# Performance work log

Measured on AMD Instinct MI355X. Metric: run time of the kernel, lower is better.

Reference implementation:

```python
import jax, jax.numpy as jnp
import numpy as np

B = 64
L_IN = 4001
L_CONV = 998  # (4001-10)//4 + 1
D = 1000
EPS = 1e-5


def _convlin(x, cw, cb, lw, lb):
    # x: (B,1,4001), cw: (1,1,10), lw: (1000,998)
    y = jax.lax.conv_general_dilated(
        x, cw, window_strides=(4,), padding='VALID',
        dimension_numbers=('NCH', 'OIH', 'NCH')) + cb[None, :, None]  # (B,1,998)
    y = y @ lw.T + lb  # (B,1,1000)
    return jax.nn.relu(y)


def setup_inputs() -> dict:
    key = jax.random.key(0)
    ks = jax.random.split(key, 24)
    f32 = jnp.float32
    inp = {
        'x': jax.random.normal(ks[0], (B, 1, L_IN), dtype=f32),
        'bn_gamma': jnp.ones((L_IN,), f32),
        'bn_beta': jnp.zeros((L_IN,), f32),
        'bn_mean': jax.random.normal(ks[1], (L_IN,), f32) * 0.1,
        'bn_var': jax.random.uniform(ks[2], (L_IN,), f32, 0.5, 1.5),
        'conv_w_q': jax.random.normal(ks[3], (1, 1, 10), f32) * 0.3,
        'conv_b_q': jax.random.normal(ks[4], (1,), f32) * 0.1,
        'lin_w_q': jax.random.normal(ks[5], (D, L_CONV), f32) * (1.0 / np.sqrt(L_CONV)),
        'lin_b_q': jax.random.normal(ks[6], (D,), f32) * 0.02,
        'conv_w_k': jax.random.normal(ks[7], (1, 1, 10), f32) * 0.3,
        'conv_b_k': jax.random.normal(ks[8], (1,), f32) * 0.1,
        'lin_w_k': jax.random.normal(ks[9], (D, L_CONV), f32) * (1.0 / np.sqrt(L_CONV)),
        'lin_b_k': jax.random.normal(ks[10], (D,), f32) * 0.02,
        'conv_w_v': jax.random.normal(ks[11], (1, 1, 10), f32) * 0.3,
        'conv_b_v': jax.random.normal(ks[12], (1,), f32) * 0.1,
        'lin_w_v': jax.random.normal(ks[13], (D, L_CONV), f32) * (1.0 / np.sqrt(L_CONV)),
        'lin_b_v': jax.random.normal(ks[14], (D,), f32) * 0.02,
        'in_proj_w': jax.random.normal(ks[15], (3, 1), f32),
        'in_proj_b': jax.random.normal(ks[16], (3,), f32) * 0.02,
        'out_proj_w': jax.random.normal(ks[17], (1, 1), f32),
        'out_proj_b': jax.random.normal(ks[18], (1,), f32) * 0.02,
        'out_w': jax.random.normal(ks[19], (D, D), f32) * (1.0 / np.sqrt(D)),
        'out_b': jax.random.normal(ks[20], (D,), f32) * 0.02,
    }
    return inp


def reference(x, bn_gamma, bn_beta, bn_mean, bn_var,
              conv_w_q, conv_b_q, lin_w_q, lin_b_q,
              conv_w_k, conv_b_k, lin_w_k, lin_b_k,
              conv_w_v, conv_b_v, lin_w_v, lin_b_v,
              in_proj_w, in_proj_b, out_proj_w, out_proj_b,
              out_w, out_b):
    # BatchNorm1d over last dim (eval mode, running stats); x: (B,1,4001)
    xn = (x - bn_mean[None, None, :]) * jax.lax.rsqrt(bn_var[None, None, :] + EPS)
    xn = xn * bn_gamma[None, None, :] + bn_beta[None, None, :]

    Q = _convlin(xn, conv_w_q, conv_b_q, lin_w_q, lin_b_q)[:, 0, :]  # (B,1000)
    K = _convlin(xn, conv_w_k, conv_b_k, lin_w_k, lin_b_k)[:, 0, :]
    V = _convlin(xn, conv_w_v, conv_b_v, lin_w_v, lin_b_v)[:, 0, :]

    # MHA with embed_dim=1, num_heads=1 -> scalar in-projections, scale = 1
    q = Q * in_proj_w[0, 0] + in_proj_b[0]  # (B,1000)
    k = K * in_proj_w[1, 0] + in_proj_b[1]
    v = V * in_proj_w[2, 0] + in_proj_b[2]

    scores = q[:, :, None] * k[:, None, :]  # (B,1000,1000)
    attn = jax.nn.softmax(scores, axis=-1)
    ctx = jnp.einsum('bqk,bk->bq', attn, v)  # (B,1000)
    ctx = ctx * out_proj_w[0, 0] + out_proj_b[0]

    out = ctx[:, None, :] @ out_w.T + out_b  # (B,1,1000)
    return out
```

## Files before the change

kernel.cpp:

```cpp
#include <hip/hip_runtime.h>
#include <math.h>

#define NB 64
#define LIN 4001
#define LC 998
#define ND 1000
#define EPSBN 1e-5f

#define CK 96
#define NCH_LIN 11
#define NCH_OUT 11

#define OFF_CONVT 0u
#define OFF_PP    191616u
#define OFF_CF    2354304u
#define OFF_OP    2418304u

__global__ __launch_bounds__(256) void k_bnconv(
    const float* __restrict__ x,
    const float* __restrict__ g, const float* __restrict__ be,
    const float* __restrict__ mu, const float* __restrict__ va,
    const float* __restrict__ cwq, const float* __restrict__ cbq,
    const float* __restrict__ cwk, const float* __restrict__ cbk,
    const float* __restrict__ cwv, const float* __restrict__ cbv,
    float* __restrict__ convT)
{
    int j = blockIdx.x * 256 + threadIdx.x;
    int b = blockIdx.y;
    if (j >= LC) return;
    const float* xb = x + (size_t)b * LIN + 4 * j;
    float aq = 0.f, ak = 0.f, av = 0.f;
#pragma unroll
    for (int t = 0; t < 10; ++t) {
        int i = 4 * j + t;
        float s  = g[i] * rsqrtf(va[i] + EPSBN);
        float xn = (xb[t] - mu[i]) * s + be[i];
        aq = fmaf(xn, cwq[t], aq);
        ak = fmaf(xn, cwk[t], ak);
        av = fmaf(xn, cwv[t], av);
    }
    convT[((size_t)0 * LC + j) * 64 + b] = aq + cbq[0];
    convT[((size_t)1 * LC + j) * 64 + b] = ak + cbk[0];
    convT[((size_t)2 * LC + j) * 64 + b] = av + cbv[0];
}

__device__ __forceinline__ void gemm_tile(
    const float* __restrict__ Asrc,
    const float* __restrict__ Brow,
    int ldB, int dgb, int j0, int jc,
    float* __restrict__ Pt,
    float* lds)
{
    float* ldsC = lds;
    float* ldsW = lds + 6144;
    int tid  = threadIdx.x;
    int lane = tid & 63;
    int w    = tid >> 6;
    int b0   = (lane & 7) << 3;
    int d0   = (lane >> 3) << 3;

    {
        const float4* src = (const float4*)Asrc;
        float4* dst = (float4*)ldsC;
        for (int t = tid; t < jc * 16; t += 256) dst[t] = src[t];
    }
    for (int idx = tid; idx < 3072; idx += 256) {
        int dd = idx / 48, j2 = idx % 48;
        int dg = dgb + dd;
        float2 v = make_float2(0.f, 0.f);
        if (dg < ND && 2 * j2 < jc)
            v = *(const float2*)(Brow + (size_t)dg * ldB + j0 + 2 * j2);
        ldsW[dd * 97 + 2 * j2]     = v.x;
        ldsW[dd * 97 + 2 * j2 + 1] = v.y;
    }
    __syncthreads();

    float acc[8][8];
#pragma unroll
    for (int i = 0; i < 8; ++i)
#pragma unroll
        for (int jx = 0; jx < 8; ++jx) acc[i][jx] = 0.f;

    int js = (jc * w) >> 2;
    int je = (jc * (w + 1)) >> 2;
    for (int jj = js; jj < je; ++jj) {
        float4 c0 = *(const float4*)(ldsC + jj * 64 + b0);
        float4 c1 = *(const float4*)(ldsC + jj * 64 + b0 + 4);
        float cv[8] = {c0.x, c0.y, c0.z, c0.w, c1.x, c1.y, c1.z, c1.w};
        float wv[8];
#pragma unroll
        for (int r = 0; r < 8; ++r) wv[r] = ldsW[(d0 + r) * 97 + jj];
#pragma unroll
        for (int i = 0; i < 8; ++i)
#pragma unroll
            for (int jx = 0; jx < 8; ++jx)
                acc[i][jx] = fmaf(cv[i], wv[jx], acc[i][jx]);
    }
    __syncthreads();

    for (int p = 0; p < 2; ++p) {
        float* red = lds + w * 2304;
#pragma unroll
        for (int i = 0; i < 8; ++i)
            *(float4*)(red + (b0 + i) * 36 + (d0 >> 1)) =
                make_float4(acc[i][4*p], acc[i][4*p+1], acc[i][4*p+2], acc[i][4*p+3]);
        __syncthreads();
        for (int t = tid; t < 512; t += 256) {
            int bb = t >> 3, gg = t & 7;
            int o = bb * 36 + 4 * gg;
            float4 a0 = *(const float4*)(lds + o);
            float4 a1 = *(const float4*)(lds + 2304 + o);
            float4 a2 = *(const float4*)(lds + 4608 + o);
            float4 a3 = *(const float4*)(lds + 6912 + o);
            float4 s;
            s.x = a0.x + a1.x + a2.x + a3.x;
            s.y = a0.y + a1.y + a2.y + a3.y;
            s.z = a0.z + a1.z + a2.z + a3.z;
            s.w = a0.w + a1.w + a2.w + a3.w;
            *(float4*)(Pt + bb * 64 + 8 * gg + 4 * p) = s;
        }
        __syncthreads();
    }
}

__global__ __launch_bounds__(256) void k_lin(
    const float* __restrict__ convT,
    const float* __restrict__ lwq, const float* __restrict__ lwk,
    const float* __restrict__ lwv,
    float* __restrict__ Pp)
{
    __shared__ float lds[12352];
    int dgb   = blockIdx.x * 64;
    int which = blockIdx.y;
    int chunk = blockIdx.z;
    int j0 = chunk * CK;
    int jc = (LC - j0 < CK) ? (LC - j0) : CK;
    const float* lw = (which == 0) ? lwq : ((which == 1) ? lwk : lwv);
    const float* Asrc = convT + ((size_t)which * LC + j0) * 64;
    float* Pt = Pp + (((size_t)chunk * 3 + which) * 16 + blockIdx.x) * 4096;
    gemm_tile(Asrc, lw, LC, dgb, j0, jc, Pt, lds);
}

__global__ __launch_bounds__(256) void k_attn(
    const float* __restrict__ Pp,
    const float* __restrict__ lbq, const float* __restrict__ lbk,
    const float* __restrict__ lbv,
    const float* __restrict__ ipw, const float* __restrict__ ipb,
    const float* __restrict__ opw, const float* __restrict__ opb,
    float* __restrict__ cfT)
{
    __shared__ float skv[2000];
    __shared__ float sql[128];
    __shared__ float sd[512];
    __shared__ float sn[512];
    __shared__ float rmax[4];
    __shared__ float rmin[4];
    const float LOG2E = 1.4426950408889634f;
    int tid  = threadIdx.x;
    int b    = blockIdx.y;
    int i0   = blockIdx.x * 128;
    int w    = tid >> 6;
    int lane = tid & 63;

    float ipw1 = ipw[1], ipb1 = ipb[1];
    float ipw2 = ipw[2], ipb2 = ipb[2];

    for (int j = tid; j < ND; j += 256) {
        int it = j >> 6, il = j & 63;
        size_t base = ((size_t)it) * 4096 + (b << 6) + il;
        float sk = 0.f, sv = 0.f;
        for (int c = 0; c < NCH_LIN; ++c) {
            sk += Pp[((size_t)(c * 3 + 1) * 16) * 4096 + base];
            sv += Pp[((size_t)(c * 3 + 2) * 16) * 4096 + base];
        }
        float yk = fmaxf(sk + lbk[j], 0.f) * ipw1 + ipb1;
        float yv = fmaxf(sv + lbv[j], 0.f) * ipw2 + ipb2;
        skv[2 * j]     = yk * LOG2E;
        skv[2 * j + 1] = yv;
    }
    if (tid < 128) {
        int i = i0 + tid;
        float sq = 0.f;
        if (i < ND) {
            int it = i >> 6, il = i & 63;
            size_t base = ((size_t)it) * 4096 + (b << 6) + il;
            for (int c = 0; c < NCH_LIN; ++c)
                sq += Pp[((size_t)(c * 3 + 0) * 16) * 4096 + base];
            sq = fmaxf(sq + lbq[i], 0.f) * ipw[0] + ipb[0];
        }
        sql[tid] = sq;
    }
    __syncthreads();

    float km = -INFINITY, kn = INFINITY;
    for (int j = tid; j < ND; j += 256) {
        float f = skv[2 * j];
        km = fmaxf(km, f);
        kn = fminf(kn, f);
    }
#pragma unroll
    for (int off = 1; off < 64; off <<= 1) {
        km = fmaxf(km, __shfl_xor(km, off));
        kn = fminf(kn, __shfl_xor(kn, off));
    }
    if (lane == 0) { rmax[w] = km; rmin[w] = kn; }
    __syncthreads();
    km = fmaxf(fmaxf(rmax[0], rmax[1]), fmaxf(rmax[2], rmax[3]));
    kn = fminf(fminf(rmin[0], rmin[1]), fminf(rmin[2], rmin[3]));

    float q0 = sql[lane];
    float q1 = sql[64 + lane];
    float m0 = (q0 >= 0.f) ? q0 * km : q0 * kn;
    float m1 = (q1 >= 0.f) ? q1 * km : q1 * kn;
    const float2* kv2 = (const float2*)skv;
    int jb = w * 250;
    float d0a = 0.f, n0a = 0.f, d1a = 0.f, n1a = 0.f;
#pragma unroll 2
    for (int jl = 0; jl < 250; ++jl) {
        float2 f = kv2[jb + jl];
        float e0 = exp2f(fmaf(q0, f.x, -m0));
        float e1 = exp2f(fmaf(q1, f.x, -m1));
        d0a += e0; n0a = fmaf(e0, f.y, n0a);
        d1a += e1; n1a = fmaf(e1, f.y, n1a);
    }
    sd[w * 128 + lane]      = d0a;
    sd[w * 128 + 64 + lane] = d1a;
    sn[w * 128 + lane]      = n0a;
    sn[w * 128 + 64 + lane] = n1a;
    __syncthreads();

    if (tid < 128) {
        int i = i0 + tid;
        if (i < ND) {
            float dt = sd[tid] + sd[128 + tid] + sd[256 + tid] + sd[384 + tid];
            float nt = sn[tid] + sn[128 + tid] + sn[256 + tid] + sn[384 + tid];
            cfT[(size_t)i * 64 + b] = (nt / dt) * opw[0] + opb[0];
        }
    }
}

__global__ __launch_bounds__(256) void k_out(
    const float* __restrict__ cfT, const float* __restrict__ W,
    float* __restrict__ Op)
{
    __shared__ float lds[12352];
    int egb   = blockIdx.x * 64;
    int chunk = blockIdx.y;
    int j0 = chunk * CK;
    int jc = (ND - j0 < CK) ? (ND - j0) : CK;
    const float* Asrc = cfT + (size_t)j0 * 64;
    float* Pt = Op + ((size_t)chunk * 16 + blockIdx.x) * 4096;
    gemm_tile(Asrc, W, ND, egb, j0, jc, Pt, lds);
}

__global__ __launch_bounds__(256) void k_fin(
    const float* __restrict__ Op, const float* __restrict__ outb,
    float* __restrict__ out)
{
    int e = blockIdx.x * 256 + threadIdx.x;
    int b = blockIdx.y;
    if (e >= ND) return;
    float s = outb[e];
    size_t cell = ((size_t)(e >> 6)) * 4096 + (b << 6) + (e & 63);
    for (int c = 0; c < NCH_OUT; ++c)
        s += Op[(size_t)c * 16 * 4096 + cell];
    out[(size_t)b * ND + e] = s;
}

extern "C" void kernel_launch(void* const* d_in, const int* in_sizes, int n_in,
                              void* d_out, int out_size, void* d_ws, size_t ws_size,
                              hipStream_t stream)
{
    const float* x    = (const float*)d_in[0];
    const float* g    = (const float*)d_in[1];
    const float* be   = (const float*)d_in[2];
    const float* mu   = (const float*)d_in[3];
    const float* va   = (const float*)d_in[4];
    const float* cwq  = (const float*)d_in[5];
    const float* cbq  = (const float*)d_in[6];
    const float* lwq  = (const float*)d_in[7];
    const float* lbq  = (const float*)d_in[8];
    const float* cwk  = (const float*)d_in[9];
    const float* cbk  = (const float*)d_in[10];
    const float* lwk  = (const float*)d_in[11];
    const float* lbk  = (const float*)d_in[12];
    const float* cwv  = (const float*)d_in[13];
    const float* cbv  = (const float*)d_in[14];
    const float* lwv  = (const float*)d_in[15];
    const float* lbv  = (const float*)d_in[16];
    const float* ipw  = (const float*)d_in[17];
    const float* ipb  = (const float*)d_in[18];
    const float* opw  = (const float*)d_in[19];
    const float* opb  = (const float*)d_in[20];
    const float* W    = (const float*)d_in[21];
    const float* outb = (const float*)d_in[22];

    float* ws    = (float*)d_ws;
    float* convT = ws + OFF_CONVT;
    float* Pp    = ws + OFF_PP;
    float* cfT   = ws + OFF_CF;
    float* Op    = ws + OFF_OP;
    float* out   = (float*)d_out;

    k_bnconv<<<dim3(4, 64), 256, 0, stream>>>(x, g, be, mu, va,
                                              cwq, cbq, cwk, cbk, cwv, cbv, convT);
    k_lin  <<<dim3(16, 3, NCH_LIN), 256, 0, stream>>>(convT, lwq, lwk, lwv, Pp);
    k_attn <<<dim3(8, 64), 256, 0, stream>>>(Pp, lbq, lbk, lbv, ipw, ipb,
                                             opw, opb, cfT);
    k_out  <<<dim3(16, NCH_OUT), 256, 0, stream>>>(cfT, W, Op);
    k_fin  <<<dim3(4, 64), 256, 0, stream>>>(Op, outb, out);
}
```

Measured before the change: 174.5 us.

## Fuse all five stages into one cooperative persistent kernel with grid syncs

Replaces the five separate kernel launches with a single cooperative kernel of 512 blocks that runs each stage and separates them with grid.sync(). The K-chunk size grows from 96 to 104, so there are 10 partial chunks instead of 11. The attention-input reduction now runs as its own grid-wide stage that writes q and the interleaved k/v into global scratch, so attention blocks no longer each redo the partial-sum reduction. The aim is to remove launch gaps and redundant reductions, at the cost of grid-barrier overhead and fewer active blocks in the GEMM stages.

```diff
diff --git a/kernel.cpp b/kernel.cpp
--- a/kernel.cpp
+++ b/kernel.cpp
@@ -1,5 +1,8 @@
 #include <hip/hip_runtime.h>
+#include <hip/hip_cooperative_groups.h>
 #include <math.h>
+
+namespace cg = cooperative_groups;
 
 #define NB 64
 #define LIN 4001
@@ -7,42 +10,28 @@
 #define ND 1000
 #define EPSBN 1e-5f
 
-#define CK 96
-#define NCH_LIN 11
-#define NCH_OUT 11
+#define CK 104
+#define NCH_LIN 10
+#define NCH_OUT 10
+#define T_LIN 480
+#define T_OUT 160
+#define GRID 512
 
 #define OFF_CONVT 0u
 #define OFF_PP    191616u
-#define OFF_CF    2354304u
-#define OFF_OP    2418304u
-
-__global__ __launch_bounds__(256) void k_bnconv(
-    const float* __restrict__ x,
-    const float* __restrict__ g, const float* __restrict__ be,
-    const float* __restrict__ mu, const float* __restrict__ va,
-    const float* __restrict__ cwq, const float* __restrict__ cbq,
-    const float* __restrict__ cwk, const float* __restrict__ cbk,
-    const float* __restrict__ cwv, const float* __restrict__ cbv,
-    float* __restrict__ convT)
-{
-    int j = blockIdx.x * 256 + threadIdx.x;
-    int b = blockIdx.y;
-    if (j >= LC) return;
-    const float* xb = x + (size_t)b * LIN + 4 * j;
-    float aq = 0.f, ak = 0.f, av = 0.f;
-#pragma unroll
-    for (int t = 0; t < 10; ++t) {
-        int i = 4 * j + t;
-        float s  = g[i] * rsqrtf(va[i] + EPSBN);
-        float xn = (xb[t] - mu[i]) * s + be[i];
-        aq = fmaf(xn, cwq[t], aq);
-        ak = fmaf(xn, cwk[t], ak);
-        av = fmaf(xn, cwv[t], av);
-    }
-    convT[((size_t)0 * LC + j) * 64 + b] = aq + cbq[0];
-    convT[((size_t)1 * LC + j) * 64 + b] = ak + cbk[0];
-    convT[((size_t)2 * LC + j) * 64 + b] = av + cbv[0];
-}
+#define OFF_Q     2157696u
+#define OFF_KV    2221696u
+#define OFF_CF    2352768u
+#define OFF_OP    2416768u
+
+struct Params {
+    const float *x, *g, *be, *mu, *va;
+    const float *cwq, *cbq, *lwq, *lbq;
+    const float *cwk, *cbk, *lwk, *lbk;
+    const float *cwv, *cbv, *lwv, *lbv;
+    const float *ipw, *ipb, *opw, *opb, *W, *outb;
+    float *convT, *Pp, *qg, *kvg, *cfT, *Op, *out;
+};
 
 __device__ __forceinline__ void gemm_tile(
     const float* __restrict__ Asrc,
@@ -52,7 +41,7 @@
     float* lds)
 {
     float* ldsC = lds;
-    float* ldsW = lds + 6144;
+    float* ldsW = lds + 6656;
     int tid  = threadIdx.x;
     int lane = tid & 63;
     int w    = tid >> 6;
@@ -64,14 +53,14 @@
         float4* dst = (float4*)ldsC;
         for (int t = tid; t < jc * 16; t += 256) dst[t] = src[t];
     }
-    for (int idx = tid; idx < 3072; idx += 256) {
-        int dd = idx / 48, j2 = idx % 48;
+    for (int idx = tid; idx < 3328; idx += 256) {
+        int dd = idx / 52, j2 = idx % 52;
         int dg = dgb + dd;
         float2 v = make_float2(0.f, 0.f);
         if (dg < ND && 2 * j2 < jc)
             v = *(const float2*)(Brow + (size_t)dg * ldB + j0 + 2 * j2);
-        ldsW[dd * 97 + 2 * j2]     = v.x;
-        ldsW[dd * 97 + 2 * j2 + 1] = v.y;
+        ldsW[dd * 105 + 2 * j2]     = v.x;
+        ldsW[dd * 105 + 2 * j2 + 1] = v.y;
     }
     __syncthreads();
 
@@ -89,7 +78,7 @@
         float cv[8] = {c0.x, c0.y, c0.z, c0.w, c1.x, c1.y, c1.z, c1.w};
         float wv[8];
 #pragma unroll
-        for (int r = 0; r < 8; ++r) wv[r] = ldsW[(d0 + r) * 97 + jj];
+        for (int r = 0; r < 8; ++r) wv[r] = ldsW[(d0 + r) * 105 + jj];
 #pragma unroll
         for (int i = 0; i < 8; ++i)
 #pragma unroll
@@ -123,190 +112,211 @@
     }
 }
 
-__global__ __launch_bounds__(256) void k_lin(
-    const float* __restrict__ convT,
-    const float* __restrict__ lwq, const float* __restrict__ lwk,
-    const float* __restrict__ lwv,
-    float* __restrict__ Pp)
+__global__ __launch_bounds__(256, 2) void k_all(Params p)
 {
-    __shared__ float lds[12352];
-    int dgb   = blockIdx.x * 64;
-    int which = blockIdx.y;
-    int chunk = blockIdx.z;
-    int j0 = chunk * CK;
-    int jc = (LC - j0 < CK) ? (LC - j0) : CK;
-    const float* lw = (which == 0) ? lwq : ((which == 1) ? lwk : lwv);
-    const float* Asrc = convT + ((size_t)which * LC + j0) * 64;
-    float* Pt = Pp + (((size_t)chunk * 3 + which) * 16 + blockIdx.x) * 4096;
-    gemm_tile(Asrc, lw, LC, dgb, j0, jc, Pt, lds);
-}
-
-__global__ __launch_bounds__(256) void k_attn(
-    const float* __restrict__ Pp,
-    const float* __restrict__ lbq, const float* __restrict__ lbk,
-    const float* __restrict__ lbv,
-    const float* __restrict__ ipw, const float* __restrict__ ipb,
-    const float* __restrict__ opw, const float* __restrict__ opb,
-    float* __restrict__ cfT)
-{
-    __shared__ float skv[2000];
-    __shared__ float sql[128];
-    __shared__ float sd[512];
-    __shared__ float sn[512];
-    __shared__ float rmax[4];
-    __shared__ float rmin[4];
-    const float LOG2E = 1.4426950408889634f;
-    int tid  = threadIdx.x;
-    int b    = blockIdx.y;
-    int i0   = blockIdx.x * 128;
-    int w    = tid >> 6;
-    int lane = tid & 63;
-
-    float ipw1 = ipw[1], ipb1 = ipb[1];
-    float ipw2 = ipw[2], ipb2 = ipb[2];
-
-    for (int j = tid; j < ND; j += 256) {
-        int it = j >> 6, il = j & 63;
-        size_t base = ((size_t)it) * 4096 + (b << 6) + il;
-        float sk = 0.f, sv = 0.f;
-        for (int c = 0; c < NCH_LIN; ++c) {
-            sk += Pp[((size_t)(c * 3 + 1) * 16) * 4096 + base];
-            sv += Pp[((size_t)(c * 3 + 2) * 16) * 4096 + base];
-        }
-        float yk = fmaxf(sk + lbk[j], 0.f) * ipw1 + ipb1;
-        float yv = fmaxf(sv + lbv[j], 0.f) * ipw2 + ipb2;
-        skv[2 * j]     = yk * LOG2E;
-        skv[2 * j + 1] = yv;
-    }
-    if (tid < 128) {
-        int i = i0 + tid;
-        float sq = 0.f;
-        if (i < ND) {
+    __shared__ float lds[13376];
+    cg::grid_group grid = cg::this_grid();
+    const int tid = threadIdx.x;
+    const int bid = blockIdx.x;
+    const int gsz = GRID * 256;
+    const int gtid = bid * 256 + tid;
+
+    {
+        int idx = gtid;
+        if (idx < LC * NB) {
+            int j = idx % LC, b = idx / LC;
+            const float* xb = p.x + (size_t)b * LIN + 4 * j;
+            float aq = 0.f, ak = 0.f, av = 0.f;
+#pragma unroll
+            for (int t = 0; t < 10; ++t) {
+                int i = 4 * j + t;
+                float s  = p.g[i] * rsqrtf(p.va[i] + EPSBN);
+                float xn = (xb[t] - p.mu[i]) * s + p.be[i];
+                aq = fmaf(xn, p.cwq[t], aq);
+                ak = fmaf(xn, p.cwk[t], ak);
+                av = fmaf(xn, p.cwv[t], av);
+            }
+            p.convT[((size_t)0 * LC + j) * 64 + b] = aq + p.cbq[0];
+            p.convT[((size_t)1 * LC + j) * 64 + b] = ak + p.cbk[0];
+            p.convT[((size_t)2 * LC + j) * 64 + b] = av + p.cbv[0];
+        }
+    }
+    grid.sync();
+
+    if (bid < T_LIN) {
+        int t = bid;
+        int dx = t & 15;
+        int which = (t >> 4) % 3;
+        int chunk = t / 48;
+        int j0 = chunk * CK;
+        int jc = (LC - j0 < CK) ? (LC - j0) : CK;
+        const float* lw = (which == 0) ? p.lwq : ((which == 1) ? p.lwk : p.lwv);
+        const float* Asrc = p.convT + ((size_t)which * LC + j0) * 64;
+        float* Pt = p.Pp + (((size_t)chunk * 3 + which) * 16 + dx) * 4096;
+        gemm_tile(Asrc, lw, LC, dx * 64, j0, jc, Pt, lds);
+    }
+    grid.sync();
+
+    {
+        int idx = gtid;
+        if (idx < NB * ND) {
+            int i = idx % ND, b = idx / ND;
             int it = i >> 6, il = i & 63;
             size_t base = ((size_t)it) * 4096 + (b << 6) + il;
-            for (int c = 0; c < NCH_LIN; ++c)
-                sq += Pp[((size_t)(c * 3 + 0) * 16) * 4096 + base];
-            sq = fmaxf(sq + lbq[i], 0.f) * ipw[0] + ipb[0];
-        }
-        sql[tid] = sq;
-    }
-    __syncthreads();
-
-    float km = -INFINITY, kn = INFINITY;
-    for (int j = tid; j < ND; j += 256) {
-        float f = skv[2 * j];
-        km = fmaxf(km, f);
-        kn = fminf(kn, f);
-    }
-#pragma unroll
-    for (int off = 1; off < 64; off <<= 1) {
-        km = fmaxf(km, __shfl_xor(km, off));
-        kn = fminf(kn, __shfl_xor(kn, off));
-    }
-    if (lane == 0) { rmax[w] = km; rmin[w] = kn; }
-    __syncthreads();
-    km = fmaxf(fmaxf(rmax[0], rmax[1]), fmaxf(rmax[2], rmax[3]));
-    kn = fminf(fminf(rmin[0], rmin[1]), fminf(rmin[2], rmin[3]));
-
-    float q0 = sql[lane];
-    float q1 = sql[64 + lane];
-    float m0 = (q0 >= 0.f) ? q0 * km : q0 * kn;
-    float m1 = (q1 >= 0.f) ? q1 * km : q1 * kn;
-    const float2* kv2 = (const float2*)skv;
-    int jb = w * 250;
-    float d0a = 0.f, n0a = 0.f, d1a = 0.f, n1a = 0.f;
+            float s0 = 0.f, s1 = 0.f, s2 = 0.f;
+            for (int c = 0; c < NCH_LIN; ++c) {
+                size_t o = ((size_t)c * 3 * 16) * 4096 + base;
+                s0 += p.Pp[o];
+                s1 += p.Pp[o + 16 * 4096];
+                s2 += p.Pp[o + 32 * 4096];
+            }
+            const float LOG2E = 1.4426950408889634f;
+            float yq = fmaxf(s0 + p.lbq[i], 0.f) * p.ipw[0] + p.ipb[0];
+            float yk = fmaxf(s1 + p.lbk[i], 0.f) * p.ipw[1] + p.ipb[1];
+            float yv = fmaxf(s2 + p.lbv[i], 0.f) * p.ipw[2] + p.ipb[2];
+            p.qg[(size_t)b * ND + i] = yq;
+            p.kvg[(size_t)b * 2048 + 2 * i]     = yk * LOG2E;
+            p.kvg[(size_t)b * 2048 + 2 * i + 1] = yv;
+        }
+    }
+    grid.sync();
+
+    {
+        float* skv  = lds;
+        float* sql  = lds + 2000;
+        float* sd   = lds + 2128;
+        float* sn   = lds + 2640;
+        float* rmax = lds + 3152;
+        float* rmin = lds + 3156;
+        int t  = bid;
+        int i0 = (t & 7) * 128;
+        int b  = t >> 3;
+        int w    = tid >> 6;
+        int lane = tid & 63;
+
+        {
+            const float4* src = (const float4*)(p.kvg + (size_t)b * 2048);
+            float4* dst = (float4*)skv;
+            for (int tt = tid; tt < 500; tt += 256) dst[tt] = src[tt];
+        }
+        if (tid < 128) {
+            int i = i0 + tid;
+            sql[tid] = (i < ND) ? p.qg[(size_t)b * ND + i] : 0.f;
+        }
+        __syncthreads();
+
+        float km = -INFINITY, kn = INFINITY;
+        for (int j = tid; j < ND; j += 256) {
+            float f = skv[2 * j];
+            km = fmaxf(km, f);
+            kn = fminf(kn, f);
+        }
+#pragma unroll
+        for (int off = 1; off < 64; off <<= 1) {
+            km = fmaxf(km, __shfl_xor(km, off));
+            kn = fminf(kn, __shfl_xor(kn, off));
+        }
+        if (lane == 0) { rmax[w] = km; rmin[w] = kn; }
+        __syncthreads();
+        km = fmaxf(fmaxf(rmax[0], rmax[1]), fmaxf(rmax[2], rmax[3]));
+        kn = fminf(fminf(rmin[0], rmin[1]), fminf(rmin[2], rmin[3]));
+
+        float q0 = sql[lane];
+        float q1 = sql[64 + lane];
+        float m0 = (q0 >= 0.f) ? q0 * km : q0 * kn;
+        float m1 = (q1 >= 0.f) ? q1 * km : q1 * kn;
+        const float2* kv2 = (const float2*)skv;
+        int jb = w * 250;
+        float d0a = 0.f, n0a = 0.f, d1a = 0.f, n1a = 0.f;
 #pragma unroll 2
-    for (int jl = 0; jl < 250; ++jl) {
-        float2 f = kv2[jb + jl];
-        float e0 = exp2f(fmaf(q0, f.x, -m0));
-        float e1 = exp2f(fmaf(q1, f.x, -m1));
-        d0a += e0; n0a = fmaf(e0, f.y, n0a);
-        d1a += e1; n1a = fmaf(e1, f.y, n1a);
-    }
-    sd[w * 128 + lane]      = d0a;
-    sd[w * 128 + 64 + lane] = d1a;
-    sn[w * 128 + lane]      = n0a;
-    sn[w * 128 + 64 + lane] = n1a;
-    __syncthreads();
-
-    if (tid < 128) {
-        int i = i0 + tid;
-        if (i < ND) {
-            float dt = sd[tid] + sd[128 + tid] + sd[256 + tid] + sd[384 + tid];
-            float nt = sn[tid] + sn[128 + tid] + sn[256 + tid] + sn[384 + tid];
-            cfT[(size_t)i * 64 + b] = (nt / dt) * opw[0] + opb[0];
-        }
-    }
-}
-
-__global__ __launch_bounds__(256) void k_out(
-    const float* __restrict__ cfT, const float* __restrict__ W,
-    float* __restrict__ Op)
-{
-    __shared__ float lds[12352];
-    int egb   = blockIdx.x * 64;
-    int chunk = blockIdx.y;
-    int j0 = chunk * CK;
-    int jc = (ND - j0 < CK) ? (ND - j0) : CK;
-    const float* Asrc = cfT + (size_t)j0 * 64;
-    float* Pt = Op + ((size_t)chunk * 16 + blockIdx.x) * 4096;
-    gemm_tile(Asrc, W, ND, egb, j0, jc, Pt, lds);
-}
-
-__global__ __launch_bounds__(256) void k_fin(
-    const float* __restrict__ Op, const float* __restrict__ outb,
-    float* __restrict__ out)
-{
-    int e = blockIdx.x * 256 + threadIdx.x;
-    int b = blockIdx.y;
-    if (e >= ND) return;
-    float s = outb[e];
-    size_t cell = ((size_t)(e >> 6)) * 4096 + (b << 6) + (e & 63);
-    for (int c = 0; c < NCH_OUT; ++c)
-        s += Op[(size_t)c * 16 * 4096 + cell];
-    out[(size_t)b * ND + e] = s;
+        for (int jl = 0; jl < 250; ++jl) {
+            float2 f = kv2[jb + jl];
+            float e0 = exp2f(fmaf(q0, f.x, -m0));
+            float e1 = exp2f(fmaf(q1, f.x, -m1));
+            d0a += e0; n0a = fmaf(e0, f.y, n0a);
+            d1a += e1; n1a = fmaf(e1, f.y, n1a);
+        }
+        sd[w * 128 + lane]      = d0a;
+        sd[w * 128 + 64 + lane] = d1a;
+        sn[w * 128 + lane]      = n0a;
+        sn[w * 128 + 64 + lane] = n1a;
+        __syncthreads();
+
+        if (tid < 128) {
+            int i = i0 + tid;
+            if (i < ND) {
+                float dt = sd[tid] + sd[128 + tid] + sd[256 + tid] + sd[384 + tid];
+                float nt = sn[tid] + sn[128 + tid] + sn[256 + tid] + sn[384 + tid];
+                p.cfT[(size_t)i * 64 + b] = (nt / dt) * p.opw[0] + p.opb[0];
+            }
+        }
+        __syncthreads();
+    }
+    grid.sync();
+
+    if (bid < T_OUT) {
+        int t = bid;
+        int dx = t & 15;
+        int chunk = t >> 4;
+        int j0 = chunk * CK;
+        int jc = (ND - j0 < CK) ? (ND - j0) : CK;
+        const float* Asrc = p.cfT + (size_t)j0 * 64;
+        float* Pt = p.Op + ((size_t)chunk * 16 + dx) * 4096;
+        gemm_tile(Asrc, p.W, ND, dx * 64, j0, jc, Pt, lds);
+    }
+    grid.sync();
+
+    {
+        int idx = gtid;
+        if (idx < NB * ND) {
+            int e = idx % ND, b = idx / ND;
+            float s = p.outb[e];
+            size_t cell = ((size_t)(e >> 6)) * 4096 + (b << 6) + (e & 63);
+            for (int c = 0; c < NCH_OUT; ++c)
+                s += p.Op[(size_t)c * 16 * 4096 + cell];
+            p.out[(size_t)b * ND + e] = s;
+        }
+    }
 }
 
 extern "C" void kernel_launch(void* const* d_in, const int* in_sizes, int n_in,
                               void* d_out, int out_size, void* d_ws, size_t ws_size,
                               hipStream_t stream)
 {
-    const float* x    = (const float*)d_in[0];
-    const float* g    = (const float*)d_in[1];
-    const float* be   = (const float*)d_in[2];
-    const float* mu   = (const float*)d_in[3];
-    const float* va   = (const float*)d_in[4];
-    const float* cwq  = (const float*)d_in[5];
-    const float* cbq  = (const float*)d_in[6];
-    const float* lwq  = (const float*)d_in[7];
-    const float* lbq  = (const float*)d_in[8];
-    const float* cwk  = (const float*)d_in[9];
-    const float* cbk  = (const float*)d_in[10];
-    const float* lwk  = (const float*)d_in[11];
-    const float* lbk  = (const float*)d_in[12];
-    const float* cwv  = (const float*)d_in[13];
-    const float* cbv  = (const float*)d_in[14];
-    const float* lwv  = (const float*)d_in[15];
-    const float* lbv  = (const float*)d_in[16];
-    const float* ipw  = (const float*)d_in[17];
-    const float* ipb  = (const float*)d_in[18];
-    const float* opw  = (const float*)d_in[19];
-    const float* opb  = (const float*)d_in[20];
-    const float* W    = (const float*)d_in[21];
-    const float* outb = (const float*)d_in[22];
-
-    float* ws    = (float*)d_ws;
-    float* convT = ws + OFF_CONVT;
-    float* Pp    = ws + OFF_PP;
-    float* cfT   = ws + OFF_CF;
-    float* Op    = ws + OFF_OP;
-    float* out   = (float*)d_out;
-
-    k_bnconv<<<dim3(4, 64), 256, 0, stream>>>(x, g, be, mu, va,
-                                              cwq, cbq, cwk, cbk, cwv, cbv, convT);
-    k_lin  <<<dim3(16, 3, NCH_LIN), 256, 0, stream>>>(convT, lwq, lwk, lwv, Pp);
-    k_attn <<<dim3(8, 64), 256, 0, stream>>>(Pp, lbq, lbk, lbv, ipw, ipb,
-                                             opw, opb, cfT);
-    k_out  <<<dim3(16, NCH_OUT), 256, 0, stream>>>(cfT, W, Op);
-    k_fin  <<<dim3(4, 64), 256, 0, stream>>>(Op, outb, out);
+    float* ws = (float*)d_ws;
+    Params p;
+    p.x    = (const float*)d_in[0];
+    p.g    = (const float*)d_in[1];
+    p.be   = (const float*)d_in[2];
+    p.mu   = (const float*)d_in[3];
+    p.va   = (const float*)d_in[4];
+    p.cwq  = (const float*)d_in[5];
+    p.cbq  = (const float*)d_in[6];
+    p.lwq  = (const float*)d_in[7];
+    p.lbq  = (const float*)d_in[8];
+    p.cwk  = (const float*)d_in[9];
+    p.cbk  = (const float*)d_in[10];
+    p.lwk  = (const float*)d_in[11];
+    p.lbk  = (const float*)d_in[12];
+    p.cwv  = (const float*)d_in[13];
+    p.cbv  = (const float*)d_in[14];
+    p.lwv  = (const float*)d_in[15];
+    p.lbv  = (const float*)d_in[16];
+    p.ipw  = (const float*)d_in[17];
+    p.ipb  = (const float*)d_in[18];
+    p.opw  = (const float*)d_in[19];
+    p.opb  = (const float*)d_in[20];
+    p.W    = (const float*)d_in[21];
+    p.outb = (const float*)d_in[22];
+    p.convT = ws + OFF_CONVT;
+    p.Pp    = ws + OFF_PP;
+    p.qg    = ws + OFF_Q;
+    p.kvg   = ws + OFF_KV;
+    p.cfT   = ws + OFF_CF;
+    p.Op    = ws + OFF_OP;
+    p.out   = (float*)d_out;
+
+    void* args[] = {&p};
+    hipLaunchCooperativeKernel((void*)k_all, dim3(GRID), dim3(256),
+                               args, 0, stream);
 }
```

After: 484.4 us. 178% more time.
